# Kernel tuning notes

Hardware: AMD Instinct MI355X
Metric: run time of the kernel (lower is better)

## Reference

```python
import jax, jax.numpy as jnp
import numpy as np

L, D, H, N, R = 4, 256, 512, 16, 8  # layers, d_model, hidden=2*d_model, state_dim, dt_rank
OUT_LEN, IN_DIM = 96, 32
EPS = 1e-5


def _layernorm(v, g, b):
    m = jnp.mean(v, axis=-1, keepdims=True)
    var = jnp.mean((v - m) ** 2, axis=-1, keepdims=True)
    return (v - m) / jnp.sqrt(var + EPS) * g + b


def _pos_encoding(T, d):
    pos = jnp.arange(T, dtype=jnp.float32)[:, None]
    div = jnp.exp(jnp.arange(0, d, 2, dtype=jnp.float32) * (-np.log(10000.0) / d))
    pe = jnp.zeros((T, d), dtype=jnp.float32)
    pe = pe.at[:, 0::2].set(jnp.sin(pos * div))
    pe = pe.at[:, 1::2].set(jnp.cos(pos * div))
    return pe


def setup_inputs() -> dict:
    key = jax.random.key(0)
    ks = jax.random.split(key, 20)
    inp = {
        "x": jax.random.normal(ks[0], (8, 1024, IN_DIM), dtype=jnp.float32),
        "emb_w": jax.random.normal(ks[1], (D, IN_DIM), dtype=jnp.float32) * 0.1,
        "emb_b": jnp.zeros((D,), dtype=jnp.float32),
        "norm_g": jnp.ones((L, D), dtype=jnp.float32),
        "norm_b": jnp.zeros((L, D), dtype=jnp.float32),
        "in_w": jax.random.normal(ks[2], (L, H, D), dtype=jnp.float32) * (1.0 / np.sqrt(D)),
        "conv_w": jax.random.normal(ks[3], (L, H, 1, 3), dtype=jnp.float32) * 0.5,
        "A_p": jax.random.normal(ks[4], (L, H, N), dtype=jnp.float32) * 0.01,
        "D_p": jnp.ones((L, H), dtype=jnp.float32),
        "dt1_w": jax.random.normal(ks[5], (L, R, H), dtype=jnp.float32) * (1.0 / np.sqrt(H)),
        "dt1_b": jnp.zeros((L, R), dtype=jnp.float32),
        "dt2_w": jax.random.normal(ks[6], (L, H, R), dtype=jnp.float32) * (1.0 / np.sqrt(R)),
        "dt2_b": jnp.zeros((L, H), dtype=jnp.float32),
        "out_w": jax.random.normal(ks[7], (L, D, H), dtype=jnp.float32) * (1.0 / np.sqrt(H)),
        "final_g": jnp.ones((D,), dtype=jnp.float32),
        "final_b": jnp.zeros((D,), dtype=jnp.float32),
        "head1_w": jax.random.normal(ks[8], (D, D), dtype=jnp.float32) * (1.0 / np.sqrt(D)),
        "head1_b": jnp.zeros((D,), dtype=jnp.float32),
        "head2_w": jax.random.normal(ks[9], (OUT_LEN, D), dtype=jnp.float32) * (1.0 / np.sqrt(D)),
        "head2_b": jnp.zeros((OUT_LEN,), dtype=jnp.float32),
    }
    return inp


def _mamba_block(h, g, b, in_w, conv_w, A_p, D_p, dt1_w, dt1_b, dt2_w, dt2_b, out_w):
    res = h
    v = _layernorm(h, g, b)            # [B,T,D]
    v = jnp.einsum('btd,hd->bth', v, in_w)  # [B,T,H]
    # depthwise conv1d, kernel 3, padding 1, groups=H
    vc = jnp.transpose(v, (0, 2, 1))   # [B,H,T]
    vc = jax.lax.conv_general_dilated(vc, conv_w, window_strides=(1,),
                                      padding=[(1, 1)], feature_group_count=H,
                                      dimension_numbers=('NCH', 'OIH', 'NCH'))
    v = jnp.transpose(jax.nn.silu(vc), (0, 2, 1))  # [B,T,H]
    dt = jax.nn.relu(jnp.einsum('bth,rh->btr', v, dt1_w) + dt1_b)
    dt = jnp.einsum('btr,hr->bth', dt, dt2_w) + dt2_b
    dt = jax.nn.softplus(dt)           # [B,T,H]
    A = -jnp.exp(A_p)                  # [H,N]
    safe_A = jnp.where(jnp.abs(A) < 1e-5, jnp.ones_like(A), A)

    B_sz = v.shape[0]
    state0 = jnp.zeros((B_sz, H, N), dtype=v.dtype)

    def step(state, inp):
        x_t, dt_t = inp  # [B,H] each
        dA = A * dt_t[..., None]            # [B,H,N]
        discA = jnp.exp(dA)
        discB = (discA - 1.0) / safe_A * dt_t[..., None]
        state = discA * state + discB * x_t[..., None]
        y = jnp.einsum('bhn,hn->bh', state, A_p) + D_p * x_t
        return state, y

    xs = (jnp.transpose(v, (1, 0, 2)), jnp.transpose(dt, (1, 0, 2)))  # [T,B,H]
    _, ys = jax.lax.scan(step, state0, xs)
    y = jnp.transpose(ys, (1, 0, 2))   # [B,T,H]
    return res + jnp.einsum('bth,dh->btd', y, out_w)


def reference(x, emb_w, emb_b, norm_g, norm_b, in_w, conv_w, A_p, D_p,
              dt1_w, dt1_b, dt2_w, dt2_b, out_w, final_g, final_b,
              head1_w, head1_b, head2_w, head2_b):
    h = jnp.einsum('bti,di->btd', x, emb_w) + emb_b  # [B,T,D]
    h = h + _pos_encoding(h.shape[1], D)[None]
    for l in range(L):
        h = _mamba_block(h, norm_g[l], norm_b[l], in_w[l], conv_w[l], A_p[l],
                         D_p[l], dt1_w[l], dt1_b[l], dt2_w[l], dt2_b[l], out_w[l])
    h = _layernorm(h, final_g, final_b)
    h = h[:, -1, :]                    # last token [B,D]
    h = jax.nn.silu(h @ head1_w.T + head1_b)
    return h @ head2_w.T + head2_b     # [B, OUT_LEN]
```

## Files before the change

### kernel.cpp

```cpp
#include <hip/hip_runtime.h>
#include <hip/hip_bf16.h>
#include <math.h>

#define BB 8
#define TT 1024
#define DD 256
#define HH 512
#define NN 16
#define RR 8
#define OUT_LEN 96
#define IN_DIM 32
#define MM (BB*TT)

#define SC 16
#define CC (TT/SC)

typedef unsigned short u16;
typedef unsigned int u32;
typedef __attribute__((ext_vector_type(8))) short short8;
typedef __attribute__((ext_vector_type(8))) unsigned short u16x8;
typedef __attribute__((ext_vector_type(4))) float float4v;

__device__ __forceinline__ u16 f2bf(float f) {
    __hip_bfloat16 h = __float2bfloat16(f);
    return *(u16*)&h;
}
__device__ __forceinline__ float bf2f(u16 u) {
    u32 v = ((u32)u) << 16;
    return *(float*)&v;
}

#define GLD_LDS16(src, dst) __builtin_amdgcn_global_load_lds( \
    (const __attribute__((address_space(1))) void*)(src),     \
    (__attribute__((address_space(3))) void*)(dst), 16, 0, 0)

#define SBAR()   asm volatile("s_barrier" ::: "memory")
#define VMCNT0() asm volatile("s_waitcnt vmcnt(0)" ::: "memory")
#define VMCNT4() asm volatile("s_waitcnt vmcnt(4)" ::: "memory")
#define VMCNT6() asm volatile("s_waitcnt vmcnt(6)" ::: "memory")

__global__ __launch_bounds__(256) void embed_ln_cvt_kernel(
    const float* __restrict__ x, const float* __restrict__ emb_w,
    const float* __restrict__ emb_b,
    const float* __restrict__ g, const float* __restrict__ b,
    float* __restrict__ h, u16* __restrict__ lnout,
    const float* __restrict__ w_in, u16* __restrict__ wbf_in,
    const float* __restrict__ w_out, u16* __restrict__ wbf_out, int nw)
{
    int bid = blockIdx.x;
    if (bid >= MM) {
        int i = (bid - MM) * 256 + threadIdx.x;
        if (i < nw) wbf_in[i] = f2bf(w_in[i]);
        else        wbf_out[i - nw] = f2bf(w_out[i - nw]);
        return;
    }

    int bt = bid;
    int d  = threadIdx.x;
    int t  = bt & (TT - 1);

    __shared__ float xs[IN_DIM];
    __shared__ float red[4], red2[4];
    if (threadIdx.x < IN_DIM) xs[threadIdx.x] = x[bt * IN_DIM + threadIdx.x];
    __syncthreads();

    const float* w = emb_w + d * IN_DIM;
    float acc = emb_b[d];
#pragma unroll
    for (int i = 0; i < IN_DIM; i++) acc = fmaf(xs[i], w[i], acc);

    int i2 = d & ~1;
    float div = __expf(-(float)i2 * 0.0359778918f);
    float arg = (float)t * div;
    float pe = (d & 1) ? __cosf(arg) : __sinf(arg);
    float val = acc + pe;
    h[bt * DD + d] = val;

    float s = val;
#pragma unroll
    for (int o = 32; o > 0; o >>= 1) s += __shfl_down(s, o);
    int lane = d & 63, wave = d >> 6;
    if (lane == 0) red[wave] = s;
    __syncthreads();
    float mean = (red[0] + red[1] + red[2] + red[3]) * (1.0f / DD);

    float c = val - mean;
    float s2 = c * c;
#pragma unroll
    for (int o = 32; o > 0; o >>= 1) s2 += __shfl_down(s2, o);
    if (lane == 0) red2[wave] = s2;
    __syncthreads();
    float var = (red2[0] + red2[1] + red2[2] + red2[3]) * (1.0f / DD);

    lnout[bt * DD + d] = f2bf(c * rsqrtf(var + 1e-5f) * g[d] + b[d]);
}

template<int BM, int BN, int OUT_BF16>
__global__ __launch_bounds__(256) void gemm_bf16(
    const u16* __restrict__ A, const u16* __restrict__ B,
    void* __restrict__ Cv, int M, int N, int K, int addC)
{
    constexpr int BK = 64;
    constexpr int MT = BM / 32;
    constexpr int NT = BN / 32;
    static_assert(BM == 128 && BN == 64, "vmcnt count assumes 6 loads/thread");

    __shared__ __align__(16) u16 Al[2][8][BM][8];
    __shared__ __align__(16) u16 Bl[2][8][BN][8];

    const int tid = threadIdx.x;
    const int bm = blockIdx.y * BM;
    const int bn = blockIdx.x * BN;
    const int wid = tid >> 6, lane = tid & 63;
    const int wm = wid >> 1, wn = wid & 1;
    const int lq = lane >> 4, lm = lane & 15;

    float4v acc[MT][NT];
#pragma unroll
    for (int i = 0; i < MT; i++)
#pragma unroll
        for (int j = 0; j < NT; j++) acc[i][j] = (float4v){0.f, 0.f, 0.f, 0.f};

#pragma unroll
    for (int it = 0; it < (8 * BM) / 256; it++) {
        int c = it * 256 + tid;
        int q = c / BM, row = c % BM;
        GLD_LDS16(A + (size_t)(bm + row) * K + q * 8, &Al[0][q][row][0]);
    }
#pragma unroll
    for (int it = 0; it < (8 * BN) / 256; it++) {
        int c = it * 256 + tid;
        int q = c / BN, row = c % BN;
        GLD_LDS16(B + (size_t)(bn + row) * K + q * 8, &Bl[0][q][row][0]);
    }

    const int nt = K / BK;
    int cur = 0;
    for (int i = 0; i < nt; i++) {
        if (i + 1 < nt) {
            int nxt = cur ^ 1;
            int k1 = (i + 1) * BK;
#pragma unroll
            for (int it = 0; it < (8 * BM) / 256; it++) {
                int c = it * 256 + tid;
                int q = c / BM, row = c % BM;
                GLD_LDS16(A + (size_t)(bm + row) * K + k1 + q * 8, &Al[nxt][q][row][0]);
            }
#pragma unroll
            for (int it = 0; it < (8 * BN) / 256; it++) {
                int c = it * 256 + tid;
                int q = c / BN, row = c % BN;
                GLD_LDS16(B + (size_t)(bn + row) * K + k1 + q * 8, &Bl[nxt][q][row][0]);
            }
            VMCNT6();
        } else {
            VMCNT0();
        }
        SBAR();

        short8 af[2][MT], bf[2][NT];
#pragma unroll
        for (int kk = 0; kk < 2; kk++) {
#pragma unroll
            for (int mt = 0; mt < MT; mt++)
                af[kk][mt] = *(const short8*)&Al[cur][kk * 4 + lq][wm * (BM / 2) + mt * 16 + lm][0];
#pragma unroll
            for (int nt2 = 0; nt2 < NT; nt2++)
                bf[kk][nt2] = *(const short8*)&Bl[cur][kk * 4 + lq][wn * (BN / 2) + nt2 * 16 + lm][0];
        }

#pragma unroll
        for (int kk = 0; kk < 2; kk++)
#pragma unroll
            for (int mt = 0; mt < MT; mt++)
#pragma unroll
                for (int nt2 = 0; nt2 < NT; nt2++)
                    acc[mt][nt2] = __builtin_amdgcn_mfma_f32_16x16x32_bf16(
                        af[kk][mt], bf[kk][nt2], acc[mt][nt2], 0, 0, 0);
        SBAR();
        cur ^= 1;
    }

#pragma unroll
    for (int mt = 0; mt < MT; mt++)
#pragma unroll
        for (int nt2 = 0; nt2 < NT; nt2++) {
            int row0 = bm + wm * (BM / 2) + mt * 16 + lq * 4;
            int col  = bn + wn * (BN / 2) + nt2 * 16 + lm;
#pragma unroll
            for (int r = 0; r < 4; r++) {
                float vv = acc[mt][nt2][r];
                if (OUT_BF16) {
                    ((u16*)Cv)[(size_t)(row0 + r) * N + col] = f2bf(vv);
                } else {
                    float* cp = (float*)Cv + (size_t)(row0 + r) * N + col;
                    if (addC) vv += *cp;
                    *cp = vv;
                }
            }
        }
}

__device__ __forceinline__ float softplus_f(float s) {
    return (s > 20.0f) ? s : __logf(1.0f + __expf(s));
}

__global__ __launch_bounds__(512, 4) void conv_scan1(
    const u16* __restrict__ vbf, const float* __restrict__ cwg,
    const float* __restrict__ w1g, const float* __restrict__ b1g,
    const float* __restrict__ dt2_w, const float* __restrict__ dt2_b,
    const float* __restrict__ A_p,
    u16* __restrict__ vsb, float* __restrict__ dtr,
    u16* __restrict__ Lst, float* __restrict__ sdt)
{
    const int c = blockIdx.x;
    const int b = blockIdx.y;
    const int tid = threadIdx.x;
    const int wave = tid >> 6, lane = tid & 63;
    const int h0 = lane * 8;

    __shared__ float w1s[RR * 2 * 256];
    __shared__ u16   a_lds[SC][HH];
    __shared__ float ds[SC * RR];

#pragma unroll
    for (int i = 0; i < 2; i++) {
        int rci = wave + i * 8;
        int r = rci >> 1, jc = rci & 1;
        float4 wv = *(const float4*)(w1g + r * HH + lane * 8 + jc * 4);
        *(float4*)&w1s[rci * 256 + lane * 4] = wv;
    }
    __syncthreads();

    const float* wp = cwg + h0 * 3;
#pragma unroll
    for (int i = 0; i < 2; i++) {
        int tr = wave + i * 8;
        int t  = c * SC + tr;
        size_t m = (size_t)b * TT + t;

        const u16* vrow = vbf + m * HH + h0;
        u16x8 x0 = *(const u16x8*)vrow;
        u16x8 xm = (t > 0)      ? *(const u16x8*)(vrow - HH) : (u16x8)(0);
        u16x8 xp = (t < TT - 1) ? *(const u16x8*)(vrow + HH) : (u16x8)(0);

        float a[8];
        u16x8 o;
#pragma unroll
        for (int j = 0; j < 8; j++) {
            float s = wp[j * 3] * bf2f(xm[j]);
            s = fmaf(wp[j * 3 + 1], bf2f(x0[j]), s);
            s = fmaf(wp[j * 3 + 2], bf2f(xp[j]), s);
            s = s / (1.0f + __expf(-s));
            a[j] = s;
            o[j] = f2bf(s);
        }
        *(u16x8*)(vsb + m * HH + h0) = o;
        *(u16x8*)&a_lds[tr][h0]      = o;

        float acc[RR];
#pragma unroll
        for (int r = 0; r < RR; r++) {
            float4 wlo = *(const float4*)&w1s[(r * 2 + 0) * 256 + lane * 4];
            float4 whi = *(const float4*)&w1s[(r * 2 + 1) * 256 + lane * 4];
            float s = a[0] * wlo.x;
            s = fmaf(a[1], wlo.y, s);
            s = fmaf(a[2], wlo.z, s);
            s = fmaf(a[3], wlo.w, s);
            s = fmaf(a[4], whi.x, s);
            s = fmaf(a[5], whi.y, s);
            s = fmaf(a[6], whi.z, s);
            s = fmaf(a[7], whi.w, s);
            acc[r] = s;
        }
#pragma unroll
        for (int r = 0; r < RR; r++) {
#pragma unroll
            for (int o2 = 1; o2 < 64; o2 <<= 1) acc[r] += __shfl_xor(acc[r], o2);
        }
        if (lane == 0) {
#pragma unroll
            for (int r = 0; r < RR; r++) acc[r] = fmaxf(acc[r] + b1g[r], 0.0f);
            *(float4*)(dtr + m * RR)     = make_float4(acc[0], acc[1], acc[2], acc[3]);
            *(float4*)(dtr + m * RR + 4) = make_float4(acc[4], acc[5], acc[6], acc[7]);
#pragma unroll
            for (int r = 0; r < RR; r++) ds[tr * RR + r] = acc[r];
        }
    }
    __syncthreads();

    const int h = tid;
    float A2[NN], invA[NN], st[NN];
    const float* ap = A_p + h * NN;
#pragma unroll
    for (int n = 0; n < NN; n++) {
        float av = -__expf(ap[n]);
        A2[n] = av * 1.44269504f;
        invA[n] = 1.0f / av;
        st[n] = 0.0f;
    }
    float w2[RR];
#pragma unroll
    for (int r = 0; r < RR; r++) w2[r] = dt2_w[h * RR + r];
    float b2 = dt2_b[h];

    float xv = bf2f(a_lds[0][h]);
    float s_dt = 0.0f;
#pragma unroll 2
    for (int t = 0; t < SC; t++) {
        float xn = (t + 1 < SC) ? bf2f(a_lds[t + 1][h]) : 0.0f;
        float s = b2;
#pragma unroll
        for (int r = 0; r < RR; r++) s = fmaf(ds[t * RR + r], w2[r], s);
        float dt = softplus_f(s);
        s_dt += dt;
        float dtx = dt * xv;
#pragma unroll
        for (int n = 0; n < NN; n++) {
            float e = __builtin_amdgcn_exp2f(A2[n] * dt);
            float u = invA[n] * dtx;
            st[n] = fmaf(e, st[n] + u, -u);
        }
        xv = xn;
    }

    size_t base = (((size_t)c * BB + b) * HH + h) * NN;
    u16x8 lo, hi;
#pragma unroll
    for (int n = 0; n < 8; n++) { lo[n] = f2bf(st[n]); hi[n] = f2bf(st[n + 8]); }
    *(u16x8*)(Lst + base)     = lo;
    *(u16x8*)(Lst + base + 8) = hi;
    sdt[((size_t)c * BB + b) * HH + h] = s_dt;
}

__global__ __launch_bounds__(256) void scan_carry_par(
    const float* __restrict__ A_p, const float* __restrict__ sdt,
    u16* __restrict__ Lst)
{
    int gw   = (blockIdx.x << 2) | (threadIdx.x >> 6);
    int lane = threadIdx.x & 63;
    int b = gw >> 9;
    int h = gw & 511;

    size_t sidx = ((size_t)lane * BB + b) * HH + h;
    float sd = sdt[sidx];
    const float* ap = A_p + h * NN;
    u16x8 Llo = *(const u16x8*)(Lst + sidx * NN);
    u16x8 Lhi = *(const u16x8*)(Lst + sidx * NN + 8);
    u16x8 Elo, Ehi;
#pragma unroll
    for (int n = 0; n < NN; n++) {
        float An = -__expf(ap[n]);
        float p  = __expf(An * sd);
        float lv = bf2f((n < 8) ? Llo[n] : Lhi[n - 8]);
#pragma unroll
        for (int d2 = 1; d2 < 64; d2 <<= 1) {
            float pp = __shfl_up(p, d2);
            float pl = __shfl_up(lv, d2);
            if (lane >= d2) { lv = fmaf(pl, p, lv); p = pp * p; }
        }
        float E = __shfl_up(lv, 1);
        if (lane == 0) E = 0.0f;
        if (n < 8) Elo[n] = f2bf(E); else Ehi[n - 8] = f2bf(E);
    }
    *(u16x8*)(Lst + sidx * NN)     = Elo;
    *(u16x8*)(Lst + sidx * NN + 8) = Ehi;
}

__global__ __launch_bounds__(512) void scan2_gemm2_ln(
    const u16* __restrict__ vsb, const float* __restrict__ dtr,
    const float* __restrict__ dt2_w, const float* __restrict__ dt2_b,
    const float* __restrict__ A_p, const float* __restrict__ D_p,
    const u16* __restrict__ carry,
    const u16* __restrict__ B,
    float* __restrict__ h,
    const float* __restrict__ g, const float* __restrict__ bb,
    u16* __restrict__ lnout, int doLN)
{
    const int bid = blockIdx.x;
    const int b   = bid >> 5;
    const int tb  = bid & 31;
    const int t0  = tb * 32;
    const int c0  = tb * 2;
    const int bm  = bid * 32;

    const int tid = threadIdx.x;
    const int wid = tid >> 6;
    const int lane = tid & 63;
    const int lq = lane >> 4, lm = lane & 15;
    const int wm = wid >> 2;
    const int wn = wid & 3;

    __shared__ __align__(16) u16 Yl[32 * 512];
    __shared__ __align__(16) u16 Bl[2][8][256][8];
    __shared__ float ds[32 * RR];
    __shared__ float rs[4][32], qs[4][32];

#pragma unroll
    for (int it = 0; it < 4; it++) {
        int cth = it * 512 + tid;
        int q = cth >> 8, row = cth & 255;
        GLD_LDS16(B + (size_t)row * 512 + q * 8, &Bl[0][q][row][0]);
    }

    if (tid < 256) {
        int tr = tid >> 3, r = tid & 7;
        ds[tid] = dtr[((size_t)b * TT + t0 + tr) * RR + r];
    }

    const int hh = tid;
    float A2[NN], invA[NN], Ap[NN], w2[RR];
    const float* ap = A_p + hh * NN;
#pragma unroll
    for (int n = 0; n < NN; n++) {
        float apv = ap[n]; Ap[n] = apv;
        float a = -__expf(apv);
        A2[n] = a * 1.44269504f; invA[n] = 1.0f / a;
    }
#pragma unroll
    for (int r = 0; r < RR; r++) w2[r] = dt2_w[hh * RR + r];
    float b2 = dt2_b[hh];
    float Dp = D_p[hh];
    __syncthreads();

#pragma unroll
    for (int cc = 0; cc < 2; cc++) {
        int cg = c0 + cc;
        float st[NN];
        size_t cbase = (((size_t)cg * BB + b) * HH + hh) * NN;
        u16x8 clo = *(const u16x8*)(carry + cbase);
        u16x8 chi = *(const u16x8*)(carry + cbase + 8);
#pragma unroll
        for (int n = 0; n < 8; n++) { st[n] = bf2f(clo[n]); st[n + 8] = bf2f(chi[n]); }

        const u16* vbase = vsb + ((size_t)b * TT + (size_t)cg * SC) * HH + hh;
        float xv = bf2f(vbase[0]);
#pragma unroll 2
        for (int t = 0; t < SC; t++) {
            float xn = (t + 1 < SC) ? bf2f(vbase[(size_t)(t + 1) * HH]) : 0.0f;
            int tr = cc * SC + t;
            float s = b2;
#pragma unroll
            for (int r = 0; r < RR; r++) s = fmaf(ds[tr * RR + r], w2[r], s);
            float dt = softplus_f(s);
            float dtx = dt * xv;
            float acc = Dp * xv;
#pragma unroll
            for (int n = 0; n < NN; n++) {
                float e = __builtin_amdgcn_exp2f(A2[n] * dt);
                float u = invA[n] * dtx;
                st[n] = fmaf(e, st[n] + u, -u);
                acc = fmaf(st[n], Ap[n], acc);
            }
            Yl[tr * 512 + (hh ^ ((tr & 7) << 3))] = f2bf(acc);
            xv = xn;
        }
    }
    __syncthreads();

    float4v acc4[4];
#pragma unroll
    for (int j = 0; j < 4; j++) acc4[j] = (float4v){0.f, 0.f, 0.f, 0.f};

    int cur = 0;
    for (int i = 0; i < 8; i++) {
        if (i + 1 < 8) {
            int nxt = cur ^ 1;
            int k1 = (i + 1) * 64;
#pragma unroll
            for (int it = 0; it < 4; it++) {
                int cth = it * 512 + tid;
                int q = cth >> 8, row = cth & 255;
                GLD_LDS16(B + (size_t)row * 512 + k1 + q * 8, &Bl[nxt][q][row][0]);
            }
            VMCNT4();
        } else {
            VMCNT0();
        }
        SBAR();

        int k0 = i * 64;
        short8 af[2], bf[2][4];
#pragma unroll
        for (int kk = 0; kk < 2; kk++) {
            int row = wm * 16 + lm;
            int kg  = (k0 >> 3) + kk * 4 + lq;
            af[kk] = *(const short8*)&Yl[row * 512 + ((kg ^ (row & 7)) << 3)];
#pragma unroll
            for (int nt = 0; nt < 4; nt++)
                bf[kk][nt] = *(const short8*)&Bl[cur][kk * 4 + lq][wn * 64 + nt * 16 + lm][0];
        }
#pragma unroll
        for (int kk = 0; kk < 2; kk++)
#pragma unroll
            for (int nt = 0; nt < 4; nt++)
                acc4[nt] = __builtin_amdgcn_mfma_f32_16x16x32_bf16(
                    af[kk], bf[kk][nt], acc4[nt], 0, 0, 0);
        SBAR();
        cur ^= 1;
    }

    float val[4][4];
    float s1[4] = {0.f, 0.f, 0.f, 0.f}, s2[4] = {0.f, 0.f, 0.f, 0.f};
#pragma unroll
    for (int r = 0; r < 4; r++) {
        int row = bm + wm * 16 + lq * 4 + r;
#pragma unroll
        for (int nt = 0; nt < 4; nt++) {
            int col = wn * 64 + nt * 16 + lm;
            float v = acc4[nt][r] + h[(size_t)row * DD + col];
            val[r][nt] = v;
            s1[r] += v;
            s2[r] = fmaf(v, v, s2[r]);
            h[(size_t)row * DD + col] = v;
        }
    }
#pragma unroll
    for (int r = 0; r < 4; r++) {
#pragma unroll
        for (int o = 1; o < 16; o <<= 1) {
            s1[r] += __shfl_xor(s1[r], o);
            s2[r] += __shfl_xor(s2[r], o);
        }
    }
    if (lm == 0) {
#pragma unroll
        for (int r = 0; r < 4; r++) {
            rs[wn][wm * 16 + lq * 4 + r] = s1[r];
            qs[wn][wm * 16 + lq * 4 + r] = s2[r];
        }
    }
    __syncthreads();

    if (doLN) {
#pragma unroll
        for (int r = 0; r < 4; r++) {
            int i = wm * 16 + lq * 4 + r;
            int row = bm + i;
            float mean = (rs[0][i] + rs[1][i] + rs[2][i] + rs[3][i]) * (1.0f / DD);
            float var  = (qs[0][i] + qs[1][i] + qs[2][i] + qs[3][i]) * (1.0f / DD) - mean * mean;
            float rstd = rsqrtf(var + 1e-5f);
#pragma unroll
            for (int nt = 0; nt < 4; nt++) {
                int col = wn * 64 + nt * 16 + lm;
                lnout[(size_t)row * DD + col] =
                    f2bf((val[r][nt] - mean) * rstd * g[col] + bb[col]);
            }
        }
    }
}

__global__ __launch_bounds__(256) void head_kernel(
    const float* __restrict__ h,
    const float* __restrict__ fg, const float* __restrict__ fb,
    const float* __restrict__ w1, const float* __restrict__ b1,
    const float* __restrict__ w2, const float* __restrict__ b2,
    float* __restrict__ out)
{
    int b = blockIdx.x;
    int d = threadIdx.x;
    __shared__ float hn[DD], s1[DD];
    __shared__ float red[4];

    float v = h[((size_t)b * TT + (TT - 1)) * DD + d];

    float s = v;
#pragma unroll
    for (int o = 32; o > 0; o >>= 1) s += __shfl_down(s, o);
    int lane = d & 63, wave = d >> 6;
    if (lane == 0) red[wave] = s;
    __syncthreads();
    float mean = (red[0] + red[1] + red[2] + red[3]) * (1.0f / DD);
    __syncthreads();

    float c = v - mean;
    float s2 = c * c;
#pragma unroll
    for (int o = 32; o > 0; o >>= 1) s2 += __shfl_down(s2, o);
    if (lane == 0) red[wave] = s2;
    __syncthreads();
    float var = (red[0] + red[1] + red[2] + red[3]) * (1.0f / DD);

    hn[d] = c * rsqrtf(var + 1e-5f) * fg[d] + fb[d];
    __syncthreads();

    float a1 = b1[d];
    const float* w1r = w1 + d * DD;
#pragma unroll 8
    for (int k = 0; k < DD; k++) a1 = fmaf(hn[k], w1r[k], a1);
    s1[d] = a1 / (1.0f + __expf(-a1));
    __syncthreads();

    if (d < OUT_LEN) {
        float a2 = b2[d];
        const float* w2r = w2 + d * DD;
#pragma unroll 8
        for (int k = 0; k < DD; k++) a2 = fmaf(s1[k], w2r[k], a2);
        out[b * OUT_LEN + d] = a2;
    }
}

extern "C" void kernel_launch(void* const* d_in, const int* in_sizes, int n_in,
                              void* d_out, int out_size, void* d_ws, size_t ws_size,
                              hipStream_t stream)
{
    (void)in_sizes; (void)n_in; (void)out_size; (void)ws_size;

    const float* x       = (const float*)d_in[0];
    const float* emb_w   = (const float*)d_in[1];
    const float* emb_b   = (const float*)d_in[2];
    const float* norm_g  = (const float*)d_in[3];
    const float* norm_b  = (const float*)d_in[4];
    const float* in_w    = (const float*)d_in[5];
    const float* conv_w  = (const float*)d_in[6];
    const float* A_p     = (const float*)d_in[7];
    const float* D_p     = (const float*)d_in[8];
    const float* dt1_w   = (const float*)d_in[9];
    const float* dt1_b   = (const float*)d_in[10];
    const float* dt2_w   = (const float*)d_in[11];
    const float* dt2_b   = (const float*)d_in[12];
    const float* out_w   = (const float*)d_in[13];
    const float* final_g = (const float*)d_in[14];
    const float* final_b = (const float*)d_in[15];
    const float* head1_w = (const float*)d_in[16];
    const float* head1_b = (const float*)d_in[17];
    const float* head2_w = (const float*)d_in[18];
    const float* head2_b = (const float*)d_in[19];
    float* outp = (float*)d_out;

    char* ws = (char*)d_ws;
    float* h     = (float*)ws;                ws += (size_t)MM * DD * 4;
    u16*   vbf   = (u16*)ws;                  ws += (size_t)MM * HH * 2;
    u16*   vsb   = (u16*)ws;                  ws += (size_t)MM * HH * 2;
    u16*   lnbuf = (u16*)ws;                  ws += (size_t)MM * DD * 2;
    float* dtr   = (float*)ws;                ws += (size_t)MM * RR * 4;
    u16*   Lst   = (u16*)ws;                  ws += (size_t)CC * BB * HH * NN * 2;
    float* sdt   = (float*)ws;                ws += (size_t)CC * BB * HH * 4;
    u16*   wbf_in  = (u16*)ws;                ws += (size_t)4 * HH * DD * 2;
    u16*   wbf_out = (u16*)ws;                ws += (size_t)4 * DD * HH * 2;

    const int NW = 4 * HH * DD;
    embed_ln_cvt_kernel<<<MM + (2 * NW) / 256, 256, 0, stream>>>(
        x, emb_w, emb_b, norm_g, norm_b, h, lnbuf,
        in_w, wbf_in, out_w, wbf_out, NW);

    for (int l = 0; l < 4; l++) {
        gemm_bf16<128, 64, 1><<<dim3(HH / 64, MM / 128), 256, 0, stream>>>(
            lnbuf, wbf_in + (size_t)l * HH * DD, vbf, MM, HH, DD, 0);

        conv_scan1<<<dim3(CC, BB), 512, 0, stream>>>(
            vbf, conv_w + (size_t)l * HH * 3,
            dt1_w + (size_t)l * RR * HH, dt1_b + l * RR,
            dt2_w + (size_t)l * HH * RR, dt2_b + l * HH,
            A_p + (size_t)l * HH * NN,
            vsb, dtr, Lst, sdt);

        scan_carry_par<<<(BB * HH) / 4, 256, 0, stream>>>(
            A_p + (size_t)l * HH * NN, sdt, Lst);

        const float* g_next = (l < 3) ? (norm_g + (l + 1) * DD) : final_g;
        const float* b_next = (l < 3) ? (norm_b + (l + 1) * DD) : final_b;
        scan2_gemm2_ln<<<MM / 32, 512, 0, stream>>>(
            vsb, dtr, dt2_w + (size_t)l * HH * RR, dt2_b + l * HH,
            A_p + (size_t)l * HH * NN, D_p + l * HH,
            Lst, wbf_out + (size_t)l * DD * HH,
            h, g_next, b_next, lnbuf, (l < 3) ? 1 : 0);
    }

    head_kernel<<<BB, 256, 0, stream>>>(h, final_g, final_b,
                                        head1_w, head1_b, head2_w, head2_b, outp);
}
```

Before: 468.1 us.

## Fuse input projection GEMM into conv/scan kernel with halo rows in LDS

Removes the standalone in-projection GEMM and computes the 16-row chunk (plus one halo row on each side, padded to 32) directly inside the conv/scan kernel via MFMA, keeping the result in LDS for the depthwise conv. This eliminates the global round trip of the bf16 projected activations and one kernel launch per layer. In exchange each block recomputes halo rows (32 rows of work for 16 useful), reloads the full weight matrix per block, uses much more LDS which can lower occupancy, and drops the min-blocks launch bound.

Result: slower. 546.5 us (+16.7%).

```diff
diff --git a/kernel.cpp b/kernel.cpp
--- a/kernel.cpp
+++ b/kernel.cpp
@@ -37,7 +37,6 @@
 #define SBAR()   asm volatile("s_barrier" ::: "memory")
 #define VMCNT0() asm volatile("s_waitcnt vmcnt(0)" ::: "memory")
 #define VMCNT4() asm volatile("s_waitcnt vmcnt(4)" ::: "memory")
-#define VMCNT6() asm volatile("s_waitcnt vmcnt(6)" ::: "memory")
 
 __global__ __launch_bounds__(256) void embed_ln_cvt_kernel(
     const float* __restrict__ x, const float* __restrict__ emb_w,
@@ -95,119 +94,15 @@
     lnout[bt * DD + d] = f2bf(c * rsqrtf(var + 1e-5f) * g[d] + b[d]);
 }
 
-template<int BM, int BN, int OUT_BF16>
-__global__ __launch_bounds__(256) void gemm_bf16(
-    const u16* __restrict__ A, const u16* __restrict__ B,
-    void* __restrict__ Cv, int M, int N, int K, int addC)
-{
-    constexpr int BK = 64;
-    constexpr int MT = BM / 32;
-    constexpr int NT = BN / 32;
-    static_assert(BM == 128 && BN == 64, "vmcnt count assumes 6 loads/thread");
-
-    __shared__ __align__(16) u16 Al[2][8][BM][8];
-    __shared__ __align__(16) u16 Bl[2][8][BN][8];
-
-    const int tid = threadIdx.x;
-    const int bm = blockIdx.y * BM;
-    const int bn = blockIdx.x * BN;
-    const int wid = tid >> 6, lane = tid & 63;
-    const int wm = wid >> 1, wn = wid & 1;
-    const int lq = lane >> 4, lm = lane & 15;
-
-    float4v acc[MT][NT];
-#pragma unroll
-    for (int i = 0; i < MT; i++)
-#pragma unroll
-        for (int j = 0; j < NT; j++) acc[i][j] = (float4v){0.f, 0.f, 0.f, 0.f};
-
-#pragma unroll
-    for (int it = 0; it < (8 * BM) / 256; it++) {
-        int c = it * 256 + tid;
-        int q = c / BM, row = c % BM;
-        GLD_LDS16(A + (size_t)(bm + row) * K + q * 8, &Al[0][q][row][0]);
-    }
-#pragma unroll
-    for (int it = 0; it < (8 * BN) / 256; it++) {
-        int c = it * 256 + tid;
-        int q = c / BN, row = c % BN;
-        GLD_LDS16(B + (size_t)(bn + row) * K + q * 8, &Bl[0][q][row][0]);
-    }
-
-    const int nt = K / BK;
-    int cur = 0;
-    for (int i = 0; i < nt; i++) {
-        if (i + 1 < nt) {
-            int nxt = cur ^ 1;
-            int k1 = (i + 1) * BK;
-#pragma unroll
-            for (int it = 0; it < (8 * BM) / 256; it++) {
-                int c = it * 256 + tid;
-                int q = c / BM, row = c % BM;
-                GLD_LDS16(A + (size_t)(bm + row) * K + k1 + q * 8, &Al[nxt][q][row][0]);
-            }
-#pragma unroll
-            for (int it = 0; it < (8 * BN) / 256; it++) {
-                int c = it * 256 + tid;
-                int q = c / BN, row = c % BN;
-                GLD_LDS16(B + (size_t)(bn + row) * K + k1 + q * 8, &Bl[nxt][q][row][0]);
-            }
-            VMCNT6();
-        } else {
-            VMCNT0();
-        }
-        SBAR();
-
-        short8 af[2][MT], bf[2][NT];
-#pragma unroll
-        for (int kk = 0; kk < 2; kk++) {
-#pragma unroll
-            for (int mt = 0; mt < MT; mt++)
-                af[kk][mt] = *(const short8*)&Al[cur][kk * 4 + lq][wm * (BM / 2) + mt * 16 + lm][0];
-#pragma unroll
-            for (int nt2 = 0; nt2 < NT; nt2++)
-                bf[kk][nt2] = *(const short8*)&Bl[cur][kk * 4 + lq][wn * (BN / 2) + nt2 * 16 + lm][0];
-        }
-
-#pragma unroll
-        for (int kk = 0; kk < 2; kk++)
-#pragma unroll
-            for (int mt = 0; mt < MT; mt++)
-#pragma unroll
-                for (int nt2 = 0; nt2 < NT; nt2++)
-                    acc[mt][nt2] = __builtin_amdgcn_mfma_f32_16x16x32_bf16(
-                        af[kk][mt], bf[kk][nt2], acc[mt][nt2], 0, 0, 0);
-        SBAR();
-        cur ^= 1;
-    }
-
-#pragma unroll
-    for (int mt = 0; mt < MT; mt++)
-#pragma unroll
-        for (int nt2 = 0; nt2 < NT; nt2++) {
-            int row0 = bm + wm * (BM / 2) + mt * 16 + lq * 4;
-            int col  = bn + wn * (BN / 2) + nt2 * 16 + lm;
-#pragma unroll
-            for (int r = 0; r < 4; r++) {
-                float vv = acc[mt][nt2][r];
-                if (OUT_BF16) {
-                    ((u16*)Cv)[(size_t)(row0 + r) * N + col] = f2bf(vv);
-                } else {
-                    float* cp = (float*)Cv + (size_t)(row0 + r) * N + col;
-                    if (addC) vv += *cp;
-                    *cp = vv;
-                }
-            }
-        }
-}
-
 __device__ __forceinline__ float softplus_f(float s) {
     return (s > 20.0f) ? s : __logf(1.0f + __expf(s));
 }
 
-__global__ __launch_bounds__(512, 4) void conv_scan1(
-    const u16* __restrict__ vbf, const float* __restrict__ cwg,
-    const float* __restrict__ w1g, const float* __restrict__ b1g,
+__global__ __launch_bounds__(512) void gemm1_conv_scan1(
+    const u16* __restrict__ lnbuf,
+    const u16* __restrict__ Bw,
+    const float* __restrict__ cwg, const float* __restrict__ w1g,
+    const float* __restrict__ b1g,
     const float* __restrict__ dt2_w, const float* __restrict__ dt2_b,
     const float* __restrict__ A_p,
     u16* __restrict__ vsb, float* __restrict__ dtr,
@@ -217,11 +112,18 @@
     const int b = blockIdx.y;
     const int tid = threadIdx.x;
     const int wave = tid >> 6, lane = tid & 63;
-    const int h0 = lane * 8;
-
+    const int lq = lane >> 4, lm = lane & 15;
+    const int wm = wave >> 2;
+    const int wn = wave & 3;
+
+    __shared__ __align__(16) u16 Al[32][32][8];
+    __shared__ __align__(16) u16 Bl[2][4][512][8];
     __shared__ float w1s[RR * 2 * 256];
+    __shared__ u16   y2[18][512];
     __shared__ u16   a_lds[SC][HH];
     __shared__ float ds[SC * RR];
+
+    const int h0 = lane * 8;
 
 #pragma unroll
     for (int i = 0; i < 2; i++) {
@@ -232,6 +134,66 @@
     }
     __syncthreads();
 
+#pragma unroll
+    for (int i = 0; i < 2; i++) {
+        int ch = i * 512 + tid;
+        int q = ch >> 5, row = ch & 31;
+        int t = c * SC - 1 + row;
+        int tc = (t < 0 || t >= TT) ? 0 : t;
+        GLD_LDS16(lnbuf + ((size_t)b * TT + tc) * DD + q * 8, &Al[q][row][0]);
+    }
+#pragma unroll
+    for (int it = 0; it < 4; it++) {
+        int ch = it * 512 + tid;
+        int q = ch >> 9, row = ch & 511;
+        GLD_LDS16(Bw + (size_t)row * DD + q * 8, &Bl[0][q][row][0]);
+    }
+
+    float4v acc[8];
+#pragma unroll
+    for (int j = 0; j < 8; j++) acc[j] = (float4v){0.f, 0.f, 0.f, 0.f};
+
+    int cur = 0;
+    for (int i = 0; i < 8; i++) {
+        if (i + 1 < 8) {
+            int nxt = cur ^ 1;
+            int k1 = (i + 1) * 32;
+#pragma unroll
+            for (int it = 0; it < 4; it++) {
+                int ch = it * 512 + tid;
+                int q = ch >> 9, row = ch & 511;
+                GLD_LDS16(Bw + (size_t)row * DD + k1 + q * 8, &Bl[nxt][q][row][0]);
+            }
+            VMCNT4();
+        } else {
+            VMCNT0();
+        }
+        SBAR();
+
+        short8 af = *(const short8*)&Al[i * 4 + lq][wm * 16 + lm][0];
+        short8 bf[8];
+#pragma unroll
+        for (int nt = 0; nt < 8; nt++)
+            bf[nt] = *(const short8*)&Bl[cur][lq][wn * 128 + nt * 16 + lm][0];
+#pragma unroll
+        for (int nt = 0; nt < 8; nt++)
+            acc[nt] = __builtin_amdgcn_mfma_f32_16x16x32_bf16(
+                af, bf[nt], acc[nt], 0, 0, 0);
+        SBAR();
+        cur ^= 1;
+    }
+
+#pragma unroll
+    for (int nt = 0; nt < 8; nt++) {
+        int col = wn * 128 + nt * 16 + lm;
+#pragma unroll
+        for (int r = 0; r < 4; r++) {
+            int row = wm * 16 + lq * 4 + r;
+            if (row < 18) y2[row][col] = f2bf(acc[nt][r]);
+        }
+    }
+    __syncthreads();
+
     const float* wp = cwg + h0 * 3;
 #pragma unroll
     for (int i = 0; i < 2; i++) {
@@ -239,10 +201,9 @@
         int t  = c * SC + tr;
         size_t m = (size_t)b * TT + t;
 
-        const u16* vrow = vbf + m * HH + h0;
-        u16x8 x0 = *(const u16x8*)vrow;
-        u16x8 xm = (t > 0)      ? *(const u16x8*)(vrow - HH) : (u16x8)(0);
-        u16x8 xp = (t < TT - 1) ? *(const u16x8*)(vrow + HH) : (u16x8)(0);
+        u16x8 x0 = *(const u16x8*)&y2[tr + 1][h0];
+        u16x8 xm = (t > 0)      ? *(const u16x8*)&y2[tr][h0]     : (u16x8)(0);
+        u16x8 xp = (t < TT - 1) ? *(const u16x8*)&y2[tr + 2][h0] : (u16x8)(0);
 
         float a[8];
         u16x8 o;
@@ -258,7 +219,7 @@
         *(u16x8*)(vsb + m * HH + h0) = o;
         *(u16x8*)&a_lds[tr][h0]      = o;
 
-        float acc[RR];
+        float acc1[RR];
 #pragma unroll
         for (int r = 0; r < RR; r++) {
             float4 wlo = *(const float4*)&w1s[(r * 2 + 0) * 256 + lane * 4];
@@ -271,20 +232,20 @@
             s = fmaf(a[5], whi.y, s);
             s = fmaf(a[6], whi.z, s);
             s = fmaf(a[7], whi.w, s);
-            acc[r] = s;
+            acc1[r] = s;
         }
 #pragma unroll
         for (int r = 0; r < RR; r++) {
 #pragma unroll
-            for (int o2 = 1; o2 < 64; o2 <<= 1) acc[r] += __shfl_xor(acc[r], o2);
+            for (int o2 = 1; o2 < 64; o2 <<= 1) acc1[r] += __shfl_xor(acc1[r], o2);
         }
         if (lane == 0) {
 #pragma unroll
-            for (int r = 0; r < RR; r++) acc[r] = fmaxf(acc[r] + b1g[r], 0.0f);
-            *(float4*)(dtr + m * RR)     = make_float4(acc[0], acc[1], acc[2], acc[3]);
-            *(float4*)(dtr + m * RR + 4) = make_float4(acc[4], acc[5], acc[6], acc[7]);
-#pragma unroll
-            for (int r = 0; r < RR; r++) ds[tr * RR + r] = acc[r];
+            for (int r = 0; r < RR; r++) acc1[r] = fmaxf(acc1[r] + b1g[r], 0.0f);
+            *(float4*)(dtr + m * RR)     = make_float4(acc1[0], acc1[1], acc1[2], acc1[3]);
+            *(float4*)(dtr + m * RR + 4) = make_float4(acc1[4], acc1[5], acc1[6], acc1[7]);
+#pragma unroll
+            for (int r = 0; r < RR; r++) ds[tr * RR + r] = acc1[r];
         }
     }
     __syncthreads();
@@ -630,7 +591,6 @@
 
     char* ws = (char*)d_ws;
     float* h     = (float*)ws;                ws += (size_t)MM * DD * 4;
-    u16*   vbf   = (u16*)ws;                  ws += (size_t)MM * HH * 2;
     u16*   vsb   = (u16*)ws;                  ws += (size_t)MM * HH * 2;
     u16*   lnbuf = (u16*)ws;                  ws += (size_t)MM * DD * 2;
     float* dtr   = (float*)ws;                ws += (size_t)MM * RR * 4;
@@ -645,11 +605,9 @@
         in_w, wbf_in, out_w, wbf_out, NW);
 
     for (int l = 0; l < 4; l++) {
-        gemm_bf16<128, 64, 1><<<dim3(HH / 64, MM / 128), 256, 0, stream>>>(
-            lnbuf, wbf_in + (size_t)l * HH * DD, vbf, MM, HH, DD, 0);
-
-        conv_scan1<<<dim3(CC, BB), 512, 0, stream>>>(
-            vbf, conv_w + (size_t)l * HH * 3,
+        gemm1_conv_scan1<<<dim3(CC, BB), 512, 0, stream>>>(
+            lnbuf, wbf_in + (size_t)l * HH * DD,
+            conv_w + (size_t)l * HH * 3,
             dt1_w + (size_t)l * RR * HH, dt1_b + l * RR,
             dt2_w + (size_t)l * HH * RR, dt2_b + l * HH,
             A_p + (size_t)l * HH * NN,
```

## Fuse head into last scan2 kernel and triple-buffer B tile loads

Applied to the files above, without the earlier changes.

The final layernorm plus MLP head now runs inside the last layer's scan2_gemm2_ln launch. It is done by the block that owns the final timestep of each batch and reuses the row statistics already in shared memory, which removes one kernel launch. The out-projection weight tile pipeline also goes from double to triple buffering, prefetching two K-slices ahead with adjusted vmcnt waits. The cost is more LDS per block (an extra 32KB buffer plus head scratch), which may lower occupancy, and a serial head tail on 8 blocks.

After: 467.9 us. Within noise of the previous version (-0.0%).

```diff
diff --git a/kernel.cpp b/kernel.cpp
--- a/kernel.cpp
+++ b/kernel.cpp
@@ -38,6 +38,7 @@
 #define VMCNT0() asm volatile("s_waitcnt vmcnt(0)" ::: "memory")
 #define VMCNT4() asm volatile("s_waitcnt vmcnt(4)" ::: "memory")
 #define VMCNT6() asm volatile("s_waitcnt vmcnt(6)" ::: "memory")
+#define VMCNT8() asm volatile("s_waitcnt vmcnt(8)" ::: "memory")
 
 __global__ __launch_bounds__(256) void embed_ln_cvt_kernel(
     const float* __restrict__ x, const float* __restrict__ emb_w,
@@ -375,7 +376,10 @@
     const u16* __restrict__ B,
     float* __restrict__ h,
     const float* __restrict__ g, const float* __restrict__ bb,
-    u16* __restrict__ lnout, int doLN)
+    u16* __restrict__ lnout, int doLN,
+    const float* __restrict__ w1h, const float* __restrict__ b1h,
+    const float* __restrict__ w2h, const float* __restrict__ b2h,
+    float* __restrict__ outp, int doHead)
 {
     const int bid = blockIdx.x;
     const int b   = bid >> 5;
@@ -392,15 +396,19 @@
     const int wn = wid & 3;
 
     __shared__ __align__(16) u16 Yl[32 * 512];
-    __shared__ __align__(16) u16 Bl[2][8][256][8];
+    __shared__ __align__(16) u16 Bl[3][8][256][8];
     __shared__ float ds[32 * RR];
     __shared__ float rs[4][32], qs[4][32];
-
-#pragma unroll
-    for (int it = 0; it < 4; it++) {
-        int cth = it * 512 + tid;
-        int q = cth >> 8, row = cth & 255;
-        GLD_LDS16(B + (size_t)row * 512 + q * 8, &Bl[0][q][row][0]);
+    __shared__ float hn[DD], sl1[DD];
+
+#pragma unroll
+    for (int pt = 0; pt < 2; pt++) {
+#pragma unroll
+        for (int it = 0; it < 4; it++) {
+            int cth = it * 512 + tid;
+            int q = cth >> 8, row = cth & 255;
+            GLD_LDS16(B + (size_t)row * 512 + pt * 64 + q * 8, &Bl[pt][q][row][0]);
+        }
     }
 
     if (tid < 256) {
@@ -462,23 +470,25 @@
 #pragma unroll
     for (int j = 0; j < 4; j++) acc4[j] = (float4v){0.f, 0.f, 0.f, 0.f};
 
-    int cur = 0;
     for (int i = 0; i < 8; i++) {
-        if (i + 1 < 8) {
-            int nxt = cur ^ 1;
-            int k1 = (i + 1) * 64;
+        if (i + 2 < 8) {
+            int nb = (i + 2) % 3;
+            int k1 = (i + 2) * 64;
 #pragma unroll
             for (int it = 0; it < 4; it++) {
                 int cth = it * 512 + tid;
                 int q = cth >> 8, row = cth & 255;
-                GLD_LDS16(B + (size_t)row * 512 + k1 + q * 8, &Bl[nxt][q][row][0]);
+                GLD_LDS16(B + (size_t)row * 512 + k1 + q * 8, &Bl[nb][q][row][0]);
             }
+            VMCNT8();
+        } else if (i + 1 < 8) {
             VMCNT4();
         } else {
             VMCNT0();
         }
         SBAR();
 
+        int cur = i % 3;
         int k0 = i * 64;
         short8 af[2], bf[2][4];
 #pragma unroll
@@ -497,7 +507,6 @@
                 acc4[nt] = __builtin_amdgcn_mfma_f32_16x16x32_bf16(
                     af[kk], bf[kk][nt], acc4[nt], 0, 0, 0);
         SBAR();
-        cur ^= 1;
     }
 
     float val[4][4];
@@ -548,55 +557,36 @@
             }
         }
     }
-}
-
-__global__ __launch_bounds__(256) void head_kernel(
-    const float* __restrict__ h,
-    const float* __restrict__ fg, const float* __restrict__ fb,
-    const float* __restrict__ w1, const float* __restrict__ b1,
-    const float* __restrict__ w2, const float* __restrict__ b2,
-    float* __restrict__ out)
-{
-    int b = blockIdx.x;
-    int d = threadIdx.x;
-    __shared__ float hn[DD], s1[DD];
-    __shared__ float red[4];
-
-    float v = h[((size_t)b * TT + (TT - 1)) * DD + d];
-
-    float s = v;
-#pragma unroll
-    for (int o = 32; o > 0; o >>= 1) s += __shfl_down(s, o);
-    int lane = d & 63, wave = d >> 6;
-    if (lane == 0) red[wave] = s;
-    __syncthreads();
-    float mean = (red[0] + red[1] + red[2] + red[3]) * (1.0f / DD);
-    __syncthreads();
-
-    float c = v - mean;
-    float s2 = c * c;
-#pragma unroll
-    for (int o = 32; o > 0; o >>= 1) s2 += __shfl_down(s2, o);
-    if (lane == 0) red[wave] = s2;
-    __syncthreads();
-    float var = (red[0] + red[1] + red[2] + red[3]) * (1.0f / DD);
-
-    hn[d] = c * rsqrtf(var + 1e-5f) * fg[d] + fb[d];
-    __syncthreads();
-
-    float a1 = b1[d];
-    const float* w1r = w1 + d * DD;
+
+    if (doHead && tb == 31) {
+        const int i31 = 31;
+        float mean = (rs[0][i31] + rs[1][i31] + rs[2][i31] + rs[3][i31]) * (1.0f / DD);
+        float var  = (qs[0][i31] + qs[1][i31] + qs[2][i31] + qs[3][i31]) * (1.0f / DD) - mean * mean;
+        float rstd = rsqrtf(var + 1e-5f);
+        const size_t row = (size_t)bm + 31;
+
+        if (tid < DD) {
+            float v = h[row * DD + tid];
+            hn[tid] = (v - mean) * rstd * g[tid] + bb[tid];
+        }
+        __syncthreads();
+
+        if (tid < DD) {
+            float a1 = b1h[tid];
+            const float* w1r = w1h + tid * DD;
 #pragma unroll 8
-    for (int k = 0; k < DD; k++) a1 = fmaf(hn[k], w1r[k], a1);
-    s1[d] = a1 / (1.0f + __expf(-a1));
-    __syncthreads();
-
-    if (d < OUT_LEN) {
-        float a2 = b2[d];
-        const float* w2r = w2 + d * DD;
+            for (int k = 0; k < DD; k++) a1 = fmaf(hn[k], w1r[k], a1);
+            sl1[tid] = a1 / (1.0f + __expf(-a1));
+        }
+        __syncthreads();
+
+        if (tid < OUT_LEN) {
+            float a2 = b2h[tid];
+            const float* w2r = w2h + tid * DD;
 #pragma unroll 8
-        for (int k = 0; k < DD; k++) a2 = fmaf(s1[k], w2r[k], a2);
-        out[b * OUT_LEN + d] = a2;
+            for (int k = 0; k < DD; k++) a2 = fmaf(sl1[k], w2r[k], a2);
+            outp[b * OUT_LEN + tid] = a2;
+        }
     }
 }
 
@@ -664,9 +654,7 @@
             vsb, dtr, dt2_w + (size_t)l * HH * RR, dt2_b + l * HH,
             A_p + (size_t)l * HH * NN, D_p + l * HH,
             Lst, wbf_out + (size_t)l * DD * HH,
-            h, g_next, b_next, lnbuf, (l < 3) ? 1 : 0);
-    }
-
-    head_kernel<<<BB, 256, 0, stream>>>(h, final_g, final_b,
-                                        head1_w, head1_b, head2_w, head2_b, outp);
-}
+            h, g_next, b_next, lnbuf, (l < 3) ? 1 : 0,
+            head1_w, head1_b, head2_w, head2_b, outp, (l == 3) ? 1 : 0);
+    }
+}
```
